# Kernel optimization log

Measured on AMD Instinct MI355X. Metric: run time of the kernel, lower is better.

The kernel has to match this reference:

```python
import jax, jax.numpy as jnp
import numpy as np

B, T, C = 2, 2048, 1024
H = 16
D = C // H  # head_dim = 64


def setup_inputs() -> dict:
    key = jax.random.key(0)
    k1, k2, k3, k4, k5 = jax.random.split(key, 5)
    s = 1.0 / np.sqrt(C)
    return {
        "x": jax.random.normal(k1, (B, T, C), dtype=jnp.float32),
        "w_qkv": jax.random.normal(k2, (C, 3 * C), dtype=jnp.float32) * s,
        "b_qkv": jax.random.normal(k3, (3 * C,), dtype=jnp.float32) * 0.01,
        "w_out": jax.random.normal(k4, (C, C), dtype=jnp.float32) * s,
        "b_out": jax.random.normal(k5, (C,), dtype=jnp.float32) * 0.01,
    }


def reference(x, w_qkv, b_qkv, w_out, b_out):
    Bx, Tx, Cx = x.shape
    qkv = x @ w_qkv + b_qkv                      # [B,T,3C]
    qkv = qkv.reshape(Bx, Tx, 3, H, D)
    q, k, v = qkv[:, :, 0], qkv[:, :, 1], qkv[:, :, 2]  # [B,T,H,D]
    # [B,H,T,T] scores with scaling
    scores = jnp.einsum("bqhd,bkhd->bhqk", q, k) / np.sqrt(D).astype(np.float32)
    causal = jnp.tril(jnp.ones((Tx, Tx), dtype=bool))
    scores = jnp.where(causal[None, None], scores, -jnp.inf)
    attn = jax.nn.softmax(scores, axis=-1)
    out = jnp.einsum("bhqk,bkhd->bqhd", attn, v).reshape(Bx, Tx, Cx)
    return out @ w_out + b_out
```

## Files before the change

### kernel.cpp

```cpp
#include <hip/hip_runtime.h>
#include <stdint.h>

typedef unsigned short u16;
typedef __attribute__((ext_vector_type(8))) short bfrag;
typedef __attribute__((ext_vector_type(4))) short bfrag4;
typedef __attribute__((ext_vector_type(4))) float f32x4;

#define MFMA_BF16 __builtin_amdgcn_mfma_f32_16x16x32_bf16

static constexpr int Bc = 2;
static constexpr int Tc = 2048;
static constexpr int Cc = 1024;
static constexpr int Hc = 16;
static constexpr int Dc = 64;
static constexpr int N3 = 3 * Cc;

__device__ __forceinline__ u16 f2bf(float f) {
    union { unsigned int i; float f; } v; v.f = f;
    unsigned int u = v.i;
    u += 0x7fffu + ((u >> 16) & 1u);
    return (u16)(u >> 16);
}
__device__ __forceinline__ unsigned int fbits(float f) {
    union { unsigned int i; float f; } v; v.f = f; return v.i;
}
__device__ __forceinline__ unsigned int pack_bf2(float hi, float lo) {
    return __builtin_amdgcn_perm(fbits(hi), fbits(lo), 0x07060302u);
}

#if __has_builtin(__builtin_amdgcn_mfma_f32_16x16x16bf16_1k)
__device__ __forceinline__ f32x4 MFMA16(bfrag4 a, bfrag4 b, f32x4 c) {
    return __builtin_amdgcn_mfma_f32_16x16x16bf16_1k(a, b, c, 0, 0, 0);
}
#elif __has_builtin(__builtin_amdgcn_mfma_f32_16x16x16_bf16)
__device__ __forceinline__ f32x4 MFMA16(bfrag4 a, bfrag4 b, f32x4 c) {
    return __builtin_amdgcn_mfma_f32_16x16x16_bf16(a, b, c, 0, 0, 0);
}
#else
__device__ __forceinline__ f32x4 MFMA16(bfrag4 a, bfrag4 b, f32x4 c) {
    bfrag a8 = {a[0], a[1], a[2], a[3], 0, 0, 0, 0};
    bfrag b8 = {b[0], b[1], b[2], b[3], 0, 0, 0, 0};
    return MFMA_BF16(a8, b8, c, 0, 0, 0);
}
#endif

__device__ __forceinline__ void async_load16(const u16* g, u16* lds) {
    __builtin_amdgcn_global_load_lds(
        (const __attribute__((address_space(1))) unsigned int*)g,
        (__attribute__((address_space(3))) unsigned int*)lds, 16, 0, 0);
}

__global__ __launch_bounds__(256) void prep(
    const float* __restrict__ x, const float* __restrict__ w_qkv,
    const float* __restrict__ w_out, u16* __restrict__ xb,
    u16* __restrict__ WqkvT, u16* __restrict__ WoutT) {
    __shared__ u16 tile[32][33];
    const int blk = blockIdx.x, tid = threadIdx.x;
    if (blk < 4096) {
        const int i = (blk * 256 + tid) * 4;
        const float4 v = *(const float4*)(x + i);
        ushort4 o;
        o.x = f2bf(v.x); o.y = f2bf(v.y); o.z = f2bf(v.z); o.w = f2bf(v.w);
        *(ushort4*)(xb + i) = o;
        return;
    }
    const int tx = tid & 31, ty = tid >> 5;
    const float* in; u16* out; int rows, cols, c0, r0;
    if (blk < 4096 + 3072) {
        const int t = blk - 4096;
        in = w_qkv; out = WqkvT; rows = 1024; cols = 3072;
        c0 = (t % 96) * 32; r0 = (t / 96) * 32;
    } else {
        const int t = blk - 7168;
        in = w_out; out = WoutT; rows = 1024; cols = 1024;
        c0 = (t & 31) * 32; r0 = (t >> 5) * 32;
    }
    for (int i = 0; i < 4; i++)
        tile[ty + 8 * i][tx] = f2bf(in[(size_t)(r0 + ty + 8 * i) * cols + c0 + tx]);
    __syncthreads();
    for (int i = 0; i < 4; i++)
        out[(size_t)(c0 + ty + 8 * i) * rows + r0 + tx] = tile[tx][ty + 8 * i];
}

__global__ void transpose_v(const u16* __restrict__ P, u16* __restrict__ Vt) {
    __shared__ u16 tile[32][33];
    const int bh = blockIdx.z, b = bh >> 4, h = bh & 15;
    const int t0 = blockIdx.x * 32, d0 = blockIdx.y * 32;
    const int tx = threadIdx.x, ty = threadIdx.y;
    const u16* src = P + (size_t)b * Tc * N3 + 2 * Cc + h * Dc;
    for (int i = 0; i < 4; i++)
        tile[ty + 8 * i][tx] = src[(size_t)(t0 + ty + 8 * i) * N3 + d0 + tx];
    __syncthreads();
    u16* dst = Vt + ((size_t)bh * Dc) * Tc;
    for (int i = 0; i < 4; i++)
        dst[(size_t)(d0 + ty + 8 * i) * Tc + t0 + tx] = tile[tx][ty + 8 * i];
}

__global__ __launch_bounds__(512, 2) void gemm_qkv(
    const u16* __restrict__ A, const u16* __restrict__ BT,
    const float* __restrict__ bias, u16* __restrict__ out,
    int M, int Nn, int K) {
    extern __shared__ __align__(16) u16 smem[];
    u16* As = smem;
    u16* Bs = smem + 3 * (128 * 32);

    const int tid  = threadIdx.x;
    const int wave = tid >> 6, lane = tid & 63;
    const int quad = lane >> 4, l16 = lane & 15;
    const int wm = wave >> 2, wn = wave & 3;
    const int m0 = blockIdx.y * 128, n0 = blockIdx.x * 384;

    f32x4 acc[4][6];
    #pragma unroll
    for (int i = 0; i < 4; i++)
        #pragma unroll
        for (int j = 0; j < 6; j++)
            acc[i][j] = (f32x4){0.f, 0.f, 0.f, 0.f};

    const int rA = lane >> 2;
    const int cA = ((lane & 3) ^ (rA & 3)) * 8;

    const u16* Ag  = A  + (size_t)(m0 + wave * 16 + rA) * K + cA;
    const u16* Bg0 = BT + (size_t)(n0 + wave * 48 + rA) * K + cA;
    u16* ldsA = As + (wave * 16) * 32;
    u16* ldsB = Bs + (wave * 48) * 32;

    const int swz8 = (quad ^ (l16 & 3)) * 8;
    int offA[4], offB[6];
    #pragma unroll
    for (int mt = 0; mt < 4; mt++)
        offA[mt] = (wm * 64 + mt * 16 + l16) * 32 + swz8;
    #pragma unroll
    for (int nt = 0; nt < 6; nt++)
        offB[nt] = (wn * 96 + nt * 16 + l16) * 32 + swz8;

    #define STAGE_Q(t, bsel)                                                   \
        {                                                                      \
            const int k0_ = (t) << 5;                                          \
            async_load16(Ag + k0_, ldsA + (bsel) * (128 * 32));                \
            _Pragma("unroll")                                                  \
            for (int j = 0; j < 3; j++)                                        \
                async_load16(Bg0 + (size_t)(j * 16) * K + k0_,                 \
                             ldsB + (bsel) * (384 * 32) + j * (16 * 32));      \
        }

    STAGE_Q(0, 0);
    STAGE_Q(1, 1);

    const int T = K >> 5;
    for (int t = 0; t < T; t++) {
        if (t + 1 < T) asm volatile("s_waitcnt vmcnt(4)" ::: "memory");
        else           asm volatile("s_waitcnt vmcnt(0)" ::: "memory");
        __builtin_amdgcn_s_barrier();
        asm volatile("" ::: "memory");
        if (t + 2 < T) { STAGE_Q(t + 2, (t + 2) % 3); }

        const u16* Ab = As + (t % 3) * (128 * 32);
        const u16* Bb = Bs + (t % 3) * (384 * 32);
        bfrag af[4], bf[6];
        #pragma unroll
        for (int mt = 0; mt < 4; mt++) af[mt] = *(const bfrag*)(Ab + offA[mt]);
        #pragma unroll
        for (int nt = 0; nt < 6; nt++) bf[nt] = *(const bfrag*)(Bb + offB[nt]);

        __builtin_amdgcn_s_setprio(1);
        #pragma unroll
        for (int mt = 0; mt < 4; mt++)
            #pragma unroll
            for (int nt = 0; nt < 6; nt++)
                acc[mt][nt] = MFMA_BF16(af[mt], bf[nt], acc[mt][nt], 0, 0, 0);
        __builtin_amdgcn_s_setprio(0);
    }
    #undef STAGE_Q

    #pragma unroll
    for (int nt = 0; nt < 6; nt++) {
        const int gn = n0 + wn * 96 + nt * 16 + l16;
        const float bv = bias[gn];
        #pragma unroll
        for (int mt = 0; mt < 4; mt++) {
            #pragma unroll
            for (int r = 0; r < 4; r++) {
                const int gm = m0 + wm * 64 + mt * 16 + quad * 4 + r;
                out[(size_t)gm * Nn + gn] = f2bf(acc[mt][nt][r] + bv);
            }
        }
    }
}

template <int MODE>
__global__ __launch_bounds__(256) void gemm_bt(
    const u16* __restrict__ A, const u16* __restrict__ BT,
    const float* __restrict__ bias, void* __restrict__ out_p,
    int M, int Nn, int K) {
    __shared__ __align__(16) u16 As[2][128 * 32];
    __shared__ __align__(16) u16 Bs[2][128 * 32];

    const int tid  = threadIdx.x;
    const int wave = tid >> 6, lane = tid & 63;
    const int quad = lane >> 4, l16 = lane & 15;
    const int wm = wave & 1, wn = wave >> 1;
    const int m0 = blockIdx.y * 128, n0 = blockIdx.x * 128;

    f32x4 acc[4][4];
    #pragma unroll
    for (int i = 0; i < 4; i++)
        #pragma unroll
        for (int j = 0; j < 4; j++)
            acc[i][j] = (f32x4){0.f, 0.f, 0.f, 0.f};

    const int rloc = 2 * (lane >> 3) + ((lane >> 2) & 1);
    const int cg   = ((lane & 3) ^ ((lane >> 3) & 3)) * 8;
    const int rk   = (l16 >> 1) & 3;
    const int rodd = (l16 & 1) * 32;

    const int T = K >> 5;
    #define STAGE(t, bsel)                                                      \
        {                                                                       \
            const int k0_ = (t) << 5;                                           \
            _Pragma("unroll")                                                   \
            for (int j = 0; j < 2; j++) {                                       \
                const int R0 = wave * 32 + j * 16;                              \
                async_load16(A  + (size_t)(m0 + R0 + rloc) * K + k0_ + cg,      \
                             &As[bsel][R0 * 32]);                               \
                async_load16(BT + (size_t)(n0 + R0 + rloc) * K + k0_ + cg,      \
                             &Bs[bsel][R0 * 32]);                               \
            }                                                                   \
        }

    STAGE(0, 0);
    for (int t = 0; t < T; t++) {
        __syncthreads();
        if (t + 1 < T) STAGE(t + 1, (t + 1) & 1);
        const u16* Ab = As[t & 1];
        const u16* Bb = Bs[t & 1];
        bfrag af[4], bf[4];
        #pragma unroll
        for (int mt = 0; mt < 4; mt++) {
            const int r = wm * 64 + mt * 16 + l16;
            af[mt] = *(const bfrag*)(Ab + (r >> 1) * 64 + rodd + (quad ^ rk) * 8);
        }
        #pragma unroll
        for (int nt = 0; nt < 4; nt++) {
            const int r = wn * 64 + nt * 16 + l16;
            bf[nt] = *(const bfrag*)(Bb + (r >> 1) * 64 + rodd + (quad ^ rk) * 8);
        }
        #pragma unroll
        for (int mt = 0; mt < 4; mt++)
            #pragma unroll
            for (int nt = 0; nt < 4; nt++)
                acc[mt][nt] = MFMA_BF16(af[mt], bf[nt], acc[mt][nt], 0, 0, 0);
    }
    #undef STAGE

    #pragma unroll
    for (int nt = 0; nt < 4; nt++) {
        const int gn = n0 + wn * 64 + nt * 16 + l16;
        const float bv = bias[gn];
        #pragma unroll
        for (int mt = 0; mt < 4; mt++) {
            #pragma unroll
            for (int r = 0; r < 4; r++) {
                const int gm = m0 + wm * 64 + mt * 16 + quad * 4 + r;
                if (MODE == 1)
                    ((u16*)out_p)[(size_t)gm * Nn + gn] = f2bf(acc[mt][nt][r] + bv);
                else
                    ((float*)out_p)[(size_t)gm * Nn + gn] = acc[mt][nt][r] + bv;
            }
        }
    }
}

__global__ __launch_bounds__(256, 4) void attn_kernel(
    const u16* __restrict__ QKVp, const u16* __restrict__ Vt,
    u16* __restrict__ Ob) {
    __shared__ __align__(16) u16 KsF[2][64 * 64];
    __shared__ __align__(16) u16 VsF[2][64 * 64];

    const int tid  = threadIdx.x;
    const int wave = tid >> 6, lane = tid & 63;
    const int quad = lane >> 4, l16 = lane & 15;

    const int bh = blockIdx.x & 31;
    const int jq = 31 - (blockIdx.x >> 5);
    const int b = bh >> 4, h = bh & 15;
    const u16* Qp = QKVp + (size_t)b * Tc * N3 + h * Dc;
    const u16* Kp = Qp + Cc;
    const u16* Vp = Vt + (size_t)bh * Dc * Tc;

    const int qw = jq * 64 + wave * 16;

    const int row8 = lane >> 3;
    const int swz  = ((lane & 7) ^ row8) * 8;
    const int pk0 = ((quad)     ^ (l16 & 7)) * 8;
    const int pk1 = ((quad + 4) ^ (l16 & 7)) * 8;

    bfrag qf0, qf1;
    {
        const u16* qp = Qp + (size_t)(qw + l16) * N3 + quad * 8;
        qf0 = *(const bfrag*)qp;
        qf1 = *(const bfrag*)(qp + 32);
    }

    float l_i = 0.f;
    f32x4 oacc[4];
    #pragma unroll
    for (int g = 0; g < 4; g++) oacc[g] = (f32x4){0.f, 0.f, 0.f, 0.f};

    #define STAGEKV(t, bsel)                                                    \
        {                                                                       \
            const int k0_ = (t) * 64;                                           \
            _Pragma("unroll")                                                   \
            for (int j = 0; j < 2; j++) {                                       \
                const int rr = wave * 16 + j * 8;                               \
                const int gr = rr + row8;                                       \
                async_load16(Kp + (size_t)(k0_ + gr) * N3 + swz,                \
                             &KsF[bsel][rr * 64]);                              \
                async_load16(Vp + (size_t)gr * Tc + k0_ + swz,                  \
                             &VsF[bsel][rr * 64]);                              \
            }                                                                   \
        }

    STAGEKV(0, 0);
    for (int t = 0; t <= jq; t++) {
        __syncthreads();
        if (t < jq) STAGEKV(t + 1, (t + 1) & 1);
        const u16* Kb = KsF[t & 1];
        const u16* Vb = VsF[t & 1];

        f32x4 s[4];
        #pragma unroll
        for (int g = 0; g < 4; g++) {
            const u16* kb = Kb + (g * 16 + l16) * 64;
            bfrag kf0 = *(const bfrag*)(kb + pk0);
            bfrag kf1 = *(const bfrag*)(kb + pk1);
            f32x4 z = (f32x4){0.f, 0.f, 0.f, 0.f};
            z = MFMA_BF16(kf0, qf0, z, 0, 0, 0);
            z = MFMA_BF16(kf1, qf1, z, 0, 0, 0);
            s[g] = z;
        }

        #pragma unroll
        for (int g = 0; g < 4; g++)
            #pragma unroll
            for (int r = 0; r < 4; r++)
                s[g][r] = __expf(s[g][r] * 0.125f);
        if (t == jq) {
            #pragma unroll
            for (int g = 0; g < 4; g++)
                #pragma unroll
                for (int r = 0; r < 4; r++)
                    if (g * 16 + quad * 4 + r > wave * 16 + l16) s[g][r] = 0.f;
        }
        #pragma unroll
        for (int g = 0; g < 4; g++)
            l_i += s[g][0] + s[g][1] + s[g][2] + s[g][3];

        #pragma unroll
        for (int g = 0; g < 4; g++) {
            union { unsigned int u[2]; bfrag4 v; } pf;
            pf.u[0] = pack_bf2(s[g][1], s[g][0]);
            pf.u[1] = pack_bf2(s[g][3], s[g][2]);
            const int vc = ((2 * g + (quad >> 1)) ^ (l16 & 7)) * 8 + (quad & 1) * 4;
            #pragma unroll
            for (int ng = 0; ng < 4; ng++) {
                const bfrag4 vf = *(const bfrag4*)(Vb + (ng * 16 + l16) * 64 + vc);
                oacc[ng] = MFMA16(vf, pf.v, oacc[ng]);
            }
        }
    }
    #undef STAGEKV

    float rs = l_i;
    rs += __shfl_xor(rs, 16);
    rs += __shfl_xor(rs, 32);
    const float inv = 1.f / rs;
    const int q = qw + l16;
    u16* orow = Ob + (size_t)(b * Tc + q) * Cc + h * Dc + quad * 4;
    #pragma unroll
    for (int ng = 0; ng < 4; ng++) {
        ushort4 o;
        o.x = f2bf(oacc[ng][0] * inv);
        o.y = f2bf(oacc[ng][1] * inv);
        o.z = f2bf(oacc[ng][2] * inv);
        o.w = f2bf(oacc[ng][3] * inv);
        *(ushort4*)(orow + ng * 16) = o;
    }
}

extern "C" void kernel_launch(void* const* d_in, const int* in_sizes, int n_in,
                              void* d_out, int out_size, void* d_ws, size_t ws_size,
                              hipStream_t stream) {
    const float* x     = (const float*)d_in[0];
    const float* w_qkv = (const float*)d_in[1];
    const float* b_qkv = (const float*)d_in[2];
    const float* w_out = (const float*)d_in[3];
    const float* b_out = (const float*)d_in[4];
    float* out = (float*)d_out;
    u16* ws  = (u16*)d_ws;

    u16* xb    = ws;
    u16* WqkvT = xb    + (size_t)4096 * 1024;
    u16* WoutT = WqkvT + (size_t)3072 * 1024;
    u16* QKVp  = WoutT + (size_t)1024 * 1024;
    u16* Vt    = QKVp  + (size_t)4096 * 3072;
    u16* Ao    = xb;

    static bool smem_set = false;
    if (!smem_set) {
        hipFuncSetAttribute(reinterpret_cast<const void*>(gemm_qkv),
                            hipFuncAttributeMaxDynamicSharedMemorySize,
                            96 * 1024);
        smem_set = true;
    }

    prep<<<8192, 256, 0, stream>>>(x, w_qkv, w_out, xb, WqkvT, WoutT);
    gemm_qkv<<<dim3(3072 / 384, 4096 / 128), 512, 96 * 1024, stream>>>(
        xb, WqkvT, b_qkv, QKVp, 4096, 3072, 1024);
    transpose_v<<<dim3(Tc / 32, Dc / 32, Bc * Hc), dim3(32, 8), 0, stream>>>(
        QKVp, Vt);
    attn_kernel<<<1024, 256, 0, stream>>>(QKVp, Vt, Ao);
    gemm_bt<0><<<dim3(1024 / 128, 4096 / 128), 256, 0, stream>>>(
        Ao, WoutT, b_out, out, 4096, 1024, 1024);
}
```

Before: 178.4 us.

## Fuse V transpose into QKV GEMM epilogue, retune output GEMM, prioritize attention MFMAs

The QKV GEMM epilogue now writes the V columns directly in transposed [b,h,d,t] layout, which removes the separate transpose_v kernel launch and its extra read/write pass over V. The output projection GEMM is rewritten to use 512 threads with a 3-stage async-load pipeline driven by explicit vmcnt waits and raised MFMA priority. The attention kernel also wraps its MFMA sections in s_setprio. The transposed V stores are 8-byte ushort4 writes strided by T, so the epilogue's global writes are less coalesced than before.

```diff
diff --git a/kernel.cpp b/kernel.cpp
--- a/kernel.cpp
+++ b/kernel.cpp
@@ -82,24 +82,10 @@
         out[(size_t)(c0 + ty + 8 * i) * rows + r0 + tx] = tile[tx][ty + 8 * i];
 }
 
-__global__ void transpose_v(const u16* __restrict__ P, u16* __restrict__ Vt) {
-    __shared__ u16 tile[32][33];
-    const int bh = blockIdx.z, b = bh >> 4, h = bh & 15;
-    const int t0 = blockIdx.x * 32, d0 = blockIdx.y * 32;
-    const int tx = threadIdx.x, ty = threadIdx.y;
-    const u16* src = P + (size_t)b * Tc * N3 + 2 * Cc + h * Dc;
-    for (int i = 0; i < 4; i++)
-        tile[ty + 8 * i][tx] = src[(size_t)(t0 + ty + 8 * i) * N3 + d0 + tx];
-    __syncthreads();
-    u16* dst = Vt + ((size_t)bh * Dc) * Tc;
-    for (int i = 0; i < 4; i++)
-        dst[(size_t)(d0 + ty + 8 * i) * Tc + t0 + tx] = tile[tx][ty + 8 * i];
-}
-
 __global__ __launch_bounds__(512, 2) void gemm_qkv(
     const u16* __restrict__ A, const u16* __restrict__ BT,
-    const float* __restrict__ bias, u16* __restrict__ out,
-    int M, int Nn, int K) {
+    const float* __restrict__ bias, u16* __restrict__ outQK,
+    u16* __restrict__ Vt, int M, int Nn, int K) {
     extern __shared__ __align__(16) u16 smem[];
     u16* As = smem;
     u16* Bs = smem + 3 * (128 * 32);
@@ -177,95 +163,117 @@
     for (int nt = 0; nt < 6; nt++) {
         const int gn = n0 + wn * 96 + nt * 16 + l16;
         const float bv = bias[gn];
-        #pragma unroll
-        for (int mt = 0; mt < 4; mt++) {
-            #pragma unroll
-            for (int r = 0; r < 4; r++) {
-                const int gm = m0 + wm * 64 + mt * 16 + quad * 4 + r;
-                out[(size_t)gm * Nn + gn] = f2bf(acc[mt][nt][r] + bv);
+        if (gn < 2 * Cc) {
+            #pragma unroll
+            for (int mt = 0; mt < 4; mt++) {
+                #pragma unroll
+                for (int r = 0; r < 4; r++) {
+                    const int gm = m0 + wm * 64 + mt * 16 + quad * 4 + r;
+                    outQK[(size_t)gm * Nn + gn] = f2bf(acc[mt][nt][r] + bv);
+                }
             }
-        }
-    }
-}
-
-template <int MODE>
-__global__ __launch_bounds__(256) void gemm_bt(
+        } else {
+            const int gnv = gn - 2 * Cc;
+            const int h = gnv >> 6, d = gnv & 63;
+            #pragma unroll
+            for (int mt = 0; mt < 4; mt++) {
+                const int gmb = m0 + wm * 64 + mt * 16 + quad * 4;
+                const int b = gmb >> 11, trow = gmb & (Tc - 1);
+                ushort4 o;
+                o.x = f2bf(acc[mt][nt][0] + bv);
+                o.y = f2bf(acc[mt][nt][1] + bv);
+                o.z = f2bf(acc[mt][nt][2] + bv);
+                o.w = f2bf(acc[mt][nt][3] + bv);
+                *(ushort4*)(Vt + ((size_t)((b * Hc + h) * Dc + d)) * Tc + trow) = o;
+            }
+        }
+    }
+}
+
+__global__ __launch_bounds__(512, 2) void gemm_out(
     const u16* __restrict__ A, const u16* __restrict__ BT,
-    const float* __restrict__ bias, void* __restrict__ out_p,
+    const float* __restrict__ bias, float* __restrict__ out,
     int M, int Nn, int K) {
-    __shared__ __align__(16) u16 As[2][128 * 32];
-    __shared__ __align__(16) u16 Bs[2][128 * 32];
+    extern __shared__ __align__(16) u16 smem[];
+    u16* As = smem;
+    u16* Bs = smem + 3 * (128 * 32);
 
     const int tid  = threadIdx.x;
     const int wave = tid >> 6, lane = tid & 63;
     const int quad = lane >> 4, l16 = lane & 15;
-    const int wm = wave & 1, wn = wave >> 1;
+    const int wm = wave >> 2, wn = wave & 3;
     const int m0 = blockIdx.y * 128, n0 = blockIdx.x * 128;
 
-    f32x4 acc[4][4];
+    f32x4 acc[4][2];
     #pragma unroll
     for (int i = 0; i < 4; i++)
         #pragma unroll
-        for (int j = 0; j < 4; j++)
+        for (int j = 0; j < 2; j++)
             acc[i][j] = (f32x4){0.f, 0.f, 0.f, 0.f};
 
-    const int rloc = 2 * (lane >> 3) + ((lane >> 2) & 1);
-    const int cg   = ((lane & 3) ^ ((lane >> 3) & 3)) * 8;
-    const int rk   = (l16 >> 1) & 3;
-    const int rodd = (l16 & 1) * 32;
+    const int rA = lane >> 2;
+    const int cA = ((lane & 3) ^ (rA & 3)) * 8;
+
+    const u16* Ag = A  + (size_t)(m0 + wave * 16 + rA) * K + cA;
+    const u16* Bg = BT + (size_t)(n0 + wave * 16 + rA) * K + cA;
+    u16* ldsA = As + (wave * 16) * 32;
+    u16* ldsB = Bs + (wave * 16) * 32;
+
+    const int swz8 = (quad ^ (l16 & 3)) * 8;
+    int offA[4], offB[2];
+    #pragma unroll
+    for (int mt = 0; mt < 4; mt++)
+        offA[mt] = (wm * 64 + mt * 16 + l16) * 32 + swz8;
+    #pragma unroll
+    for (int nt = 0; nt < 2; nt++)
+        offB[nt] = (wn * 32 + nt * 16 + l16) * 32 + swz8;
+
+    #define STAGE_O(t, bsel)                                                   \
+        {                                                                      \
+            const int k0_ = (t) << 5;                                          \
+            async_load16(Ag + k0_, ldsA + (bsel) * (128 * 32));                \
+            async_load16(Bg + k0_, ldsB + (bsel) * (128 * 32));                \
+        }
+
+    STAGE_O(0, 0);
+    STAGE_O(1, 1);
 
     const int T = K >> 5;
-    #define STAGE(t, bsel)                                                      \
-        {                                                                       \
-            const int k0_ = (t) << 5;                                           \
-            _Pragma("unroll")                                                   \
-            for (int j = 0; j < 2; j++) {                                       \
-                const int R0 = wave * 32 + j * 16;                              \
-                async_load16(A  + (size_t)(m0 + R0 + rloc) * K + k0_ + cg,      \
-                             &As[bsel][R0 * 32]);                               \
-                async_load16(BT + (size_t)(n0 + R0 + rloc) * K + k0_ + cg,      \
-                             &Bs[bsel][R0 * 32]);                               \
-            }                                                                   \
-        }
-
-    STAGE(0, 0);
     for (int t = 0; t < T; t++) {
-        __syncthreads();
-        if (t + 1 < T) STAGE(t + 1, (t + 1) & 1);
-        const u16* Ab = As[t & 1];
-        const u16* Bb = Bs[t & 1];
-        bfrag af[4], bf[4];
-        #pragma unroll
-        for (int mt = 0; mt < 4; mt++) {
-            const int r = wm * 64 + mt * 16 + l16;
-            af[mt] = *(const bfrag*)(Ab + (r >> 1) * 64 + rodd + (quad ^ rk) * 8);
-        }
-        #pragma unroll
-        for (int nt = 0; nt < 4; nt++) {
-            const int r = wn * 64 + nt * 16 + l16;
-            bf[nt] = *(const bfrag*)(Bb + (r >> 1) * 64 + rodd + (quad ^ rk) * 8);
-        }
+        if (t + 1 < T) asm volatile("s_waitcnt vmcnt(2)" ::: "memory");
+        else           asm volatile("s_waitcnt vmcnt(0)" ::: "memory");
+        __builtin_amdgcn_s_barrier();
+        asm volatile("" ::: "memory");
+        if (t + 2 < T) { STAGE_O(t + 2, (t + 2) % 3); }
+
+        const u16* Ab = As + (t % 3) * (128 * 32);
+        const u16* Bb = Bs + (t % 3) * (128 * 32);
+        bfrag af[4], bf[2];
+        #pragma unroll
+        for (int mt = 0; mt < 4; mt++) af[mt] = *(const bfrag*)(Ab + offA[mt]);
+        #pragma unroll
+        for (int nt = 0; nt < 2; nt++) bf[nt] = *(const bfrag*)(Bb + offB[nt]);
+
+        __builtin_amdgcn_s_setprio(1);
         #pragma unroll
         for (int mt = 0; mt < 4; mt++)
             #pragma unroll
-            for (int nt = 0; nt < 4; nt++)
+            for (int nt = 0; nt < 2; nt++)
                 acc[mt][nt] = MFMA_BF16(af[mt], bf[nt], acc[mt][nt], 0, 0, 0);
-    }
-    #undef STAGE
-
-    #pragma unroll
-    for (int nt = 0; nt < 4; nt++) {
-        const int gn = n0 + wn * 64 + nt * 16 + l16;
+        __builtin_amdgcn_s_setprio(0);
+    }
+    #undef STAGE_O
+
+    #pragma unroll
+    for (int nt = 0; nt < 2; nt++) {
+        const int gn = n0 + wn * 32 + nt * 16 + l16;
         const float bv = bias[gn];
         #pragma unroll
         for (int mt = 0; mt < 4; mt++) {
             #pragma unroll
             for (int r = 0; r < 4; r++) {
                 const int gm = m0 + wm * 64 + mt * 16 + quad * 4 + r;
-                if (MODE == 1)
-                    ((u16*)out_p)[(size_t)gm * Nn + gn] = f2bf(acc[mt][nt][r] + bv);
-                else
-                    ((float*)out_p)[(size_t)gm * Nn + gn] = acc[mt][nt][r] + bv;
+                out[(size_t)gm * Nn + gn] = acc[mt][nt][r] + bv;
             }
         }
     }
@@ -329,6 +337,7 @@
         const u16* Vb = VsF[t & 1];
 
         f32x4 s[4];
+        __builtin_amdgcn_s_setprio(1);
         #pragma unroll
         for (int g = 0; g < 4; g++) {
             const u16* kb = Kb + (g * 16 + l16) * 64;
@@ -339,6 +348,7 @@
             z = MFMA_BF16(kf1, qf1, z, 0, 0, 0);
             s[g] = z;
         }
+        __builtin_amdgcn_s_setprio(0);
 
         #pragma unroll
         for (int g = 0; g < 4; g++)
@@ -356,6 +366,7 @@
         for (int g = 0; g < 4; g++)
             l_i += s[g][0] + s[g][1] + s[g][2] + s[g][3];
 
+        __builtin_amdgcn_s_setprio(1);
         #pragma unroll
         for (int g = 0; g < 4; g++) {
             union { unsigned int u[2]; bfrag4 v; } pf;
@@ -368,6 +379,7 @@
                 oacc[ng] = MFMA16(vf, pf.v, oacc[ng]);
             }
         }
+        __builtin_amdgcn_s_setprio(0);
     }
     #undef STAGEKV
 
@@ -411,15 +423,16 @@
         hipFuncSetAttribute(reinterpret_cast<const void*>(gemm_qkv),
                             hipFuncAttributeMaxDynamicSharedMemorySize,
                             96 * 1024);
+        hipFuncSetAttribute(reinterpret_cast<const void*>(gemm_out),
+                            hipFuncAttributeMaxDynamicSharedMemorySize,
+                            48 * 1024);
         smem_set = true;
     }
 
     prep<<<8192, 256, 0, stream>>>(x, w_qkv, w_out, xb, WqkvT, WoutT);
     gemm_qkv<<<dim3(3072 / 384, 4096 / 128), 512, 96 * 1024, stream>>>(
-        xb, WqkvT, b_qkv, QKVp, 4096, 3072, 1024);
-    transpose_v<<<dim3(Tc / 32, Dc / 32, Bc * Hc), dim3(32, 8), 0, stream>>>(
-        QKVp, Vt);
+        xb, WqkvT, b_qkv, QKVp, Vt, 4096, 3072, 1024);
     attn_kernel<<<1024, 256, 0, stream>>>(QKVp, Vt, Ao);
-    gemm_bt<0><<<dim3(1024 / 128, 4096 / 128), 256, 0, stream>>>(
+    gemm_out<<<dim3(1024 / 128, 4096 / 128), 512, 48 * 1024, stream>>>(
         Ao, WoutT, b_out, out, 4096, 1024, 1024);
 }
```

New measurement: 177.7 us. No clear change (-0.4%).
